# Kernel tuning notes

Measured on AMD Instinct MI355X. Metric: run time of the kernel, lower is better.

The kernel has to match this reference:

```python
import jax, jax.numpy as jnp
import numpy as np

B, S, C, H = 8, 8192, 512, 128


def setup_inputs() -> dict:
    key = jax.random.key(0)
    k1, k2 = jax.random.split(key)
    x = jax.random.normal(k1, (B, S, C), dtype=jnp.float32)
    # nn.Linear default init: U(-1/sqrt(fan_in), 1/sqrt(fan_in))
    bound = 1.0 / np.sqrt(C)
    W = jax.random.uniform(k2, (C, H), dtype=jnp.float32, minval=-bound, maxval=bound)
    b = jnp.zeros((H,), dtype=jnp.float32)
    return {"x": x, "W": W, "b": b}


def reference(x, W, b):
    # block = identity; attn = Linear(C->H) then Softmax over sequence dim (dim=1)
    logits = jnp.einsum("bsc,ch->bsh", x, W) + b          # [B, S, H]
    a = jax.nn.softmax(logits, axis=1)                     # softmax over S
    ctx = jnp.einsum("bsh,bsc->bhc", a, x)                 # a^T @ x  -> [B, H, C]
    return jnp.einsum("bsh,bhc->bsc", a, ctx)              # a @ (a^T @ x)
```

## Files before the change

kernel.cpp:

```cpp
#include <hip/hip_runtime.h>

typedef float  f32x4 __attribute__((ext_vector_type(4)));
typedef short  s16x8 __attribute__((ext_vector_type(8)));
typedef unsigned short u16;

#define OFF_E     0ULL
#define OFF_ET    16777216ULL
#define OFF_EPART 33554432ULL
#define OFF_GT    50331648ULL
#define OFF_WT    51380224ULL
#define OFF_ZP    51511296ULL
#define OFF_RZ2   51773440ULL
#define WS_NEED   51777536ULL

__device__ __forceinline__ u16 f2bf(float f) {
  unsigned u = __float_as_uint(f);
  return (u16)((u + 0x8000u) >> 16);
}
__device__ __forceinline__ unsigned pack2(float a, float b) {
  unsigned ua = __float_as_uint(a), ub = __float_as_uint(b);
  return ((ua + 0x8000u) >> 16) | ((ub + 0x8000u) & 0xffff0000u);
}

__global__ __launch_bounds__(256) void k_wt(const float* __restrict__ W,
                                            u16* __restrict__ Wt) {
  int idx = blockIdx.x * 256 + threadIdx.x;
  int h = idx & 127, c = idx >> 7;
  Wt[h * 512 + c] = f2bf(W[c * 128 + h]);
}

__global__ __launch_bounds__(256) void k_logits_e(
    const float* __restrict__ x, const u16* __restrict__ Wt,
    u16* __restrict__ e, u16* __restrict__ eT, float* __restrict__ zpart) {
  __shared__ __align__(16) u16 sm[128 * 128];
  __shared__ float zs[512];
  u16* lA = sm;
  u16* lB = sm + 8192;
  const int tid = threadIdx.x;
  const int lane = tid & 63, wave = tid >> 6;
  const int l15 = lane & 15, quad = lane >> 4;
  const int mt = blockIdx.x;
  const int rowBase = mt << 7;

  f32x4 acc[2][8];
#pragma unroll
  for (int i = 0; i < 2; ++i)
#pragma unroll
    for (int j = 0; j < 8; ++j) acc[i][j] = (f32x4){0.f, 0.f, 0.f, 0.f};

  for (int kt = 0; kt < 8; ++kt) {
    const int k0 = kt << 6;
    if (kt) __syncthreads();
    {
      const int q = tid & 3, rb = tid >> 2;
#pragma unroll
      for (int rep = 0; rep < 2; ++rep) {
        const int r = rb + rep * 64;
        const float* src = x + (size_t)(rowBase + r) * 512 + k0 + q * 4;
#pragma unroll
        for (int j = 0; j < 4; ++j) {
          f32x4 v = *(const f32x4*)(src + j * 16);
          const int chunk = (2 * j + (q >> 1)) ^ (r & 7);
          unsigned* dst = (unsigned*)&lA[r * 64 + chunk * 8 + (q & 1) * 4];
          dst[0] = pack2(v[0], v[1]);
          dst[1] = pack2(v[2], v[3]);
        }
      }
    }
    {
      const int oct = tid & 7, rb = tid >> 3;
#pragma unroll
      for (int rep = 0; rep < 4; ++rep) {
        const int r = rb + rep * 32;
        s16x8 v = *(const s16x8*)(Wt + r * 512 + k0 + oct * 8);
        *(s16x8*)&lB[r * 64 + ((oct ^ (r & 7)) * 8)] = v;
      }
    }
    __syncthreads();
#pragma unroll
    for (int kk = 0; kk < 2; ++kk) {
      s16x8 af[2], bf[8];
#pragma unroll
      for (int i = 0; i < 2; ++i) {
        const int r = wave * 32 + i * 16 + l15;
        af[i] = *(const s16x8*)&lA[r * 64 + (((kk * 4 + quad) ^ (r & 7)) * 8)];
      }
#pragma unroll
      for (int j = 0; j < 8; ++j) {
        const int r = j * 16 + l15;
        bf[j] = *(const s16x8*)&lB[r * 64 + (((kk * 4 + quad) ^ (r & 7)) * 8)];
      }
#pragma unroll
      for (int i = 0; i < 2; ++i)
#pragma unroll
        for (int j = 0; j < 8; ++j)
          acc[i][j] = __builtin_amdgcn_mfma_f32_16x16x32_bf16(af[i], bf[j], acc[i][j], 0, 0, 0);
    }
  }

  float ex[2][8][4];
  float cs[8];
#pragma unroll
  for (int j = 0; j < 8; ++j) cs[j] = 0.f;
#pragma unroll
  for (int i = 0; i < 2; ++i)
#pragma unroll
    for (int j = 0; j < 8; ++j)
#pragma unroll
      for (int rr = 0; rr < 4; ++rr) {
        float l = acc[i][j][rr];
        l = fminf(fmaxf(l, -30.f), 30.f);
        float t = __expf(l);
        ex[i][j][rr] = t;
        cs[j] += t;
      }
#pragma unroll
  for (int j = 0; j < 8; ++j) {
    cs[j] += __shfl_xor(cs[j], 16);
    cs[j] += __shfl_xor(cs[j], 32);
  }
  if (quad == 0) {
#pragma unroll
    for (int j = 0; j < 8; ++j) zs[wave * 128 + j * 16 + l15] = cs[j];
  }
  __syncthreads();

#pragma unroll
  for (int i = 0; i < 2; ++i)
#pragma unroll
    for (int j = 0; j < 8; ++j)
#pragma unroll
      for (int rr = 0; rr < 4; ++rr) {
        int s = wave * 32 + i * 16 + quad * 4 + rr;
        int h = j * 16 + l15;
        sm[s * 128 + (((h >> 3) ^ (s & 15)) * 8) + (h & 7)] = f2bf(ex[i][j][rr]);
      }
  if (tid < 128)
    zpart[mt * 128 + tid] = zs[tid] + zs[128 + tid] + zs[256 + tid] + zs[384 + tid];
  __syncthreads();

  {
    int s = tid >> 1;
#pragma unroll
    for (int i = 0; i < 8; ++i) {
      int c = (tid & 1) * 8 + i;
      s16x8 v = *(const s16x8*)&sm[s * 128 + ((c ^ (s & 15)) * 8)];
      *(s16x8*)(e + (size_t)(rowBase + s) * 128 + c * 8) = v;
    }
  }
  {
    int ck = tid & 15, hb = tid >> 4;
    int b = mt >> 6;
    int sBase = (mt & 63) << 7;
#pragma unroll
    for (int pass = 0; pass < 8; ++pass) {
      int h = hb + pass * 16;
      s16x8 v;
#pragma unroll
      for (int j = 0; j < 8; ++j) {
        int s = ck * 8 + j;
        v[j] = (short)sm[s * 128 + (((h >> 3) ^ (s & 15)) * 8) + (h & 7)];
      }
      *(s16x8*)(eT + (size_t)(b * 128 + h) * 8192 + sBase + ck * 8) = v;
    }
  }
}

__global__ __launch_bounds__(256) void k_zmerge(const float* __restrict__ zpart,
                                                float* __restrict__ rz2) {
  int gid = blockIdx.x * 256 + threadIdx.x;
  int b = gid >> 7, h = gid & 127;
  float z = 0.f;
  for (int i = 0; i < 64; ++i) z += zpart[(b * 64 + i) * 128 + h];
  rz2[gid] = 1.0f / (z * z);
}

__global__ __launch_bounds__(256) void k_E(const float* __restrict__ x,
                                           const u16* __restrict__ eT,
                                           float* __restrict__ Epart) {
  __shared__ __align__(16) u16 lA[128 * 64];
  __shared__ __align__(16) u16 lB[64 * 64];
  const int tid = threadIdx.x;
  const int lane = tid & 63, wave = tid >> 6;
  const int l15 = lane & 15, quad = lane >> 4;
  const int nt = blockIdx.x;
  const int b = blockIdx.y;
  const int kc = blockIdx.z;

  f32x4 acc[2][4];
#pragma unroll
  for (int i = 0; i < 2; ++i)
#pragma unroll
    for (int j = 0; j < 4; ++j) acc[i][j] = (f32x4){0.f, 0.f, 0.f, 0.f};

  for (int kt = 0; kt < 16; ++kt) {
    const int sb = kc * 1024 + kt * 64;
    if (kt) __syncthreads();
    {
      const int oct = tid & 7, rb = tid >> 3;
#pragma unroll
      for (int rep = 0; rep < 4; ++rep) {
        const int r = rb + rep * 32;
        s16x8 v = *(const s16x8*)(eT + (size_t)(b * 128 + r) * 8192 + sb + oct * 8);
        *(s16x8*)&lA[r * 64 + ((oct ^ (r & 7)) * 8)] = v;
      }
    }
    {
      const int cq = tid & 15, sp = tid >> 4;
#pragma unroll
      for (int p = 0; p < 2; ++p) {
        const int sl = p * 32 + sp * 2;
        const float* src = x + (size_t)(b * 8192 + sb + sl) * 512 + nt * 64 + cq * 4;
        f32x4 v0 = *(const f32x4*)src;
        f32x4 v1 = *(const f32x4*)(src + 512);
#pragma unroll
        for (int i = 0; i < 4; ++i) {
          const int c = cq * 4 + i;
          const int chunk = ((sl >> 3) & 7) ^ ((c >> 3) & 7);
          *(unsigned*)&lB[c * 64 + chunk * 8 + (sl & 7)] = pack2(v0[i], v1[i]);
        }
      }
    }
    __syncthreads();
#pragma unroll
    for (int kk = 0; kk < 2; ++kk) {
      s16x8 af[2], bf[4];
#pragma unroll
      for (int i = 0; i < 2; ++i) {
        const int r = wave * 32 + i * 16 + l15;
        af[i] = *(const s16x8*)&lA[r * 64 + (((kk * 4 + quad) ^ (r & 7)) * 8)];
      }
#pragma unroll
      for (int j = 0; j < 4; ++j) {
        const int n = j * 16 + l15;
        bf[j] = *(const s16x8*)&lB[n * 64 + (((kk * 4 + quad) ^ ((n >> 3) & 7)) * 8)];
      }
#pragma unroll
      for (int i = 0; i < 2; ++i)
#pragma unroll
        for (int j = 0; j < 4; ++j)
          acc[i][j] = __builtin_amdgcn_mfma_f32_16x16x32_bf16(af[i], bf[j], acc[i][j], 0, 0, 0);
    }
  }
  float* dst = Epart + (size_t)(kc * 8 + b) * 128 * 512 + nt * 64;
#pragma unroll
  for (int i = 0; i < 2; ++i)
#pragma unroll
    for (int j = 0; j < 4; ++j)
#pragma unroll
      for (int rr = 0; rr < 4; ++rr) {
        int h = wave * 32 + i * 16 + quad * 4 + rr;
        int c = j * 16 + l15;
        dst[(size_t)h * 512 + c] = acc[i][j][rr];
      }
}

__global__ __launch_bounds__(256) void k_G(const float* __restrict__ Epart,
                                           const float* __restrict__ rz2,
                                           u16* __restrict__ Gt) {
  int idx = blockIdx.x * 256 + threadIdx.x;
  int c = idx & 511, h = (idx >> 9) & 127, b = idx >> 16;
  float s = 0.f;
#pragma unroll
  for (int p = 0; p < 8; ++p) s += Epart[((size_t)(p * 8 + b) * 128 + h) * 512 + c];
  Gt[(size_t)(b * 512 + c) * 128 + h] = f2bf(s * rz2[b * 128 + h]);
}

__global__ __launch_bounds__(256) void k_out(const u16* __restrict__ e,
                                             const u16* __restrict__ Gt,
                                             float* __restrict__ out) {
  __shared__ __align__(16) u16 lA[128 * 128];
  __shared__ __align__(16) u16 lB[128 * 128];
  const int tid = threadIdx.x;
  const int lane = tid & 63, wave = tid >> 6;
  const int l15 = lane & 15, quad = lane >> 4;
  const int st = blockIdx.x;
  const int b = blockIdx.y;

  {
    const int hx = tid & 15, rb = tid >> 4;
#pragma unroll
    for (int pass = 0; pass < 8; ++pass) {
      const int r = rb + pass * 16;
      s16x8 v = *(const s16x8*)(e + (size_t)(b * 8192 + st * 128 + r) * 128 + hx * 8);
      *(s16x8*)&lA[r * 128 + ((hx ^ (r & 15)) * 8)] = v;
    }
  }
  for (int ct = 0; ct < 4; ++ct) {
    __syncthreads();
    {
      const int hx = tid & 15, rb = tid >> 4;
#pragma unroll
      for (int pass = 0; pass < 8; ++pass) {
        const int r = rb + pass * 16;
        s16x8 v = *(const s16x8*)(Gt + (size_t)(b * 512 + ct * 128 + r) * 128 + hx * 8);
        *(s16x8*)&lB[r * 128 + ((hx ^ (r & 15)) * 8)] = v;
      }
    }
    __syncthreads();
    f32x4 acc[2][8];
#pragma unroll
    for (int i = 0; i < 2; ++i)
#pragma unroll
      for (int j = 0; j < 8; ++j) acc[i][j] = (f32x4){0.f, 0.f, 0.f, 0.f};
#pragma unroll
    for (int kk = 0; kk < 4; ++kk) {
      s16x8 af[2], bf[8];
#pragma unroll
      for (int i = 0; i < 2; ++i) {
        const int r = wave * 32 + i * 16 + l15;
        af[i] = *(const s16x8*)&lA[r * 128 + (((kk * 4 + quad) ^ (r & 15)) * 8)];
      }
#pragma unroll
      for (int j = 0; j < 8; ++j) {
        const int n = j * 16 + l15;
        bf[j] = *(const s16x8*)&lB[n * 128 + (((kk * 4 + quad) ^ (n & 15)) * 8)];
      }
#pragma unroll
      for (int i = 0; i < 2; ++i)
#pragma unroll
        for (int j = 0; j < 8; ++j)
          acc[i][j] = __builtin_amdgcn_mfma_f32_16x16x32_bf16(af[i], bf[j], acc[i][j], 0, 0, 0);
    }
#pragma unroll
    for (int i = 0; i < 2; ++i)
#pragma unroll
      for (int j = 0; j < 8; ++j)
#pragma unroll
        for (int rr = 0; rr < 4; ++rr) {
          int s = wave * 32 + i * 16 + quad * 4 + rr;
          int c = j * 16 + l15;
          out[(size_t)(b * 8192 + st * 128 + s) * 512 + ct * 128 + c] = acc[i][j][rr];
        }
  }
}

extern "C" void kernel_launch(void* const* d_in, const int* in_sizes, int n_in,
                              void* d_out, int out_size, void* d_ws, size_t ws_size,
                              hipStream_t stream) {
  if (ws_size < (size_t)WS_NEED) return;
  const float* x = (const float*)d_in[0];
  const float* W = (const float*)d_in[1];
  float* out = (float*)d_out;
  char* ws = (char*)d_ws;
  u16* e = (u16*)(ws + OFF_E);
  u16* eT = (u16*)(ws + OFF_ET);
  float* Epart = (float*)(ws + OFF_EPART);
  u16* Gt = (u16*)(ws + OFF_GT);
  u16* Wt = (u16*)(ws + OFF_WT);
  float* zpart = (float*)(ws + OFF_ZP);
  float* rz2 = (float*)(ws + OFF_RZ2);

  k_wt<<<256, 256, 0, stream>>>(W, Wt);
  k_logits_e<<<512, 256, 0, stream>>>(x, Wt, e, eT, zpart);
  k_zmerge<<<4, 256, 0, stream>>>(zpart, rz2);
  k_E<<<dim3(8, 8, 8), 256, 0, stream>>>(x, eT, Epart);
  k_G<<<2048, 256, 0, stream>>>(Epart, rz2, Gt);
  k_out<<<dim3(64, 8), 256, 0, stream>>>(e, Gt, out);
}
```

Baseline: 306.6 us.

## Pre-transpose x to bf16 and retile the a^T·x GMEM kernel

Adds a kernel that converts x to a bf16 transposed layout [B, C, S] so that k_E loads both operands as contiguous 16-byte vectors, with no per-element fp32-to-bf16 packing or scattered LDS stores. k_E now computes 128x128 output tiles (x rows by h) over 16 split-K chunks instead of 128x64 over 8, and writes Epart in [c, h] order. k_G reduces 16 partials with vectorized loads and stores packed bf16. The cost is an extra full pass over x (read 128MB fp32, write 64MB bf16) and a larger workspace.

```diff
diff --git a/kernel.cpp b/kernel.cpp
--- a/kernel.cpp
+++ b/kernel.cpp
@@ -7,11 +7,12 @@
 #define OFF_E     0ULL
 #define OFF_ET    16777216ULL
 #define OFF_EPART 33554432ULL
-#define OFF_GT    50331648ULL
-#define OFF_WT    51380224ULL
-#define OFF_ZP    51511296ULL
-#define OFF_RZ2   51773440ULL
-#define WS_NEED   51777536ULL
+#define OFF_XT    67108864ULL
+#define OFF_GT    134217728ULL
+#define OFF_WT    135266304ULL
+#define OFF_ZP    135397376ULL
+#define OFF_RZ2   135659520ULL
+#define WS_NEED   135663616ULL
 
 __device__ __forceinline__ u16 f2bf(float f) {
   unsigned u = __float_as_uint(f);
@@ -27,6 +28,39 @@
   int idx = blockIdx.x * 256 + threadIdx.x;
   int h = idx & 127, c = idx >> 7;
   Wt[h * 512 + c] = f2bf(W[c * 128 + h]);
+}
+
+__global__ __launch_bounds__(256) void k_xT(const float* __restrict__ x,
+                                            u16* __restrict__ xT) {
+  const int tid = threadIdx.x;
+  const int sc = blockIdx.x;
+  const int b  = blockIdx.y;
+  const int rq = tid & 15;
+  const int cseg = tid >> 4;
+  const int s0 = sc * 64 + rq * 4;
+#pragma unroll
+  for (int p = 0; p < 2; ++p) {
+    const int c0 = cseg * 32 + p * 16;
+    const float* src = x + ((size_t)(b * 8192 + s0) * 512 + c0);
+    f32x4 r0[4], r1[4], r2[4], r3[4];
+#pragma unroll
+    for (int j = 0; j < 4; ++j) {
+      r0[j] = *(const f32x4*)(src + j * 4);
+      r1[j] = *(const f32x4*)(src + 512 + j * 4);
+      r2[j] = *(const f32x4*)(src + 1024 + j * 4);
+      r3[j] = *(const f32x4*)(src + 1536 + j * 4);
+    }
+#pragma unroll
+    for (int j = 0; j < 4; ++j)
+#pragma unroll
+      for (int i = 0; i < 4; ++i) {
+        const int c = c0 + j * 4 + i;
+        unsigned lo = pack2(r0[j][i], r1[j][i]);
+        unsigned hi = pack2(r2[j][i], r3[j][i]);
+        unsigned long long vv = (unsigned long long)lo | ((unsigned long long)hi << 32);
+        *(unsigned long long*)(xT + ((size_t)(b * 512 + c) * 8192 + s0)) = vv;
+      }
+  }
 }
 
 __global__ __launch_bounds__(256) void k_logits_e(
@@ -175,11 +209,11 @@
   rz2[gid] = 1.0f / (z * z);
 }
 
-__global__ __launch_bounds__(256) void k_E(const float* __restrict__ x,
+__global__ __launch_bounds__(256) void k_E(const u16* __restrict__ xT,
                                            const u16* __restrict__ eT,
                                            float* __restrict__ Epart) {
   __shared__ __align__(16) u16 lA[128 * 64];
-  __shared__ __align__(16) u16 lB[64 * 64];
+  __shared__ __align__(16) u16 lB[128 * 64];
   const int tid = threadIdx.x;
   const int lane = tid & 63, wave = tid >> 6;
   const int l15 = lane & 15, quad = lane >> 4;
@@ -187,71 +221,57 @@
   const int b = blockIdx.y;
   const int kc = blockIdx.z;
 
-  f32x4 acc[2][4];
-#pragma unroll
-  for (int i = 0; i < 2; ++i)
-#pragma unroll
-    for (int j = 0; j < 4; ++j) acc[i][j] = (f32x4){0.f, 0.f, 0.f, 0.f};
-
-  for (int kt = 0; kt < 16; ++kt) {
-    const int sb = kc * 1024 + kt * 64;
+  f32x4 acc[2][8];
+#pragma unroll
+  for (int i = 0; i < 2; ++i)
+#pragma unroll
+    for (int j = 0; j < 8; ++j) acc[i][j] = (f32x4){0.f, 0.f, 0.f, 0.f};
+
+  for (int kt = 0; kt < 8; ++kt) {
+    const int sb = kc * 512 + kt * 64;
     if (kt) __syncthreads();
     {
       const int oct = tid & 7, rb = tid >> 3;
 #pragma unroll
       for (int rep = 0; rep < 4; ++rep) {
         const int r = rb + rep * 32;
-        s16x8 v = *(const s16x8*)(eT + (size_t)(b * 128 + r) * 8192 + sb + oct * 8);
-        *(s16x8*)&lA[r * 64 + ((oct ^ (r & 7)) * 8)] = v;
-      }
-    }
-    {
-      const int cq = tid & 15, sp = tid >> 4;
-#pragma unroll
-      for (int p = 0; p < 2; ++p) {
-        const int sl = p * 32 + sp * 2;
-        const float* src = x + (size_t)(b * 8192 + sb + sl) * 512 + nt * 64 + cq * 4;
-        f32x4 v0 = *(const f32x4*)src;
-        f32x4 v1 = *(const f32x4*)(src + 512);
-#pragma unroll
-        for (int i = 0; i < 4; ++i) {
-          const int c = cq * 4 + i;
-          const int chunk = ((sl >> 3) & 7) ^ ((c >> 3) & 7);
-          *(unsigned*)&lB[c * 64 + chunk * 8 + (sl & 7)] = pack2(v0[i], v1[i]);
-        }
+        s16x8 va = *(const s16x8*)(xT + (size_t)(b * 512 + nt * 128 + r) * 8192 + sb + oct * 8);
+        *(s16x8*)&lA[r * 64 + ((oct ^ (r & 7)) * 8)] = va;
+        s16x8 vb = *(const s16x8*)(eT + (size_t)(b * 128 + r) * 8192 + sb + oct * 8);
+        *(s16x8*)&lB[r * 64 + ((oct ^ (r & 7)) * 8)] = vb;
       }
     }
     __syncthreads();
 #pragma unroll
     for (int kk = 0; kk < 2; ++kk) {
-      s16x8 af[2], bf[4];
+      s16x8 af[2], bf[8];
 #pragma unroll
       for (int i = 0; i < 2; ++i) {
         const int r = wave * 32 + i * 16 + l15;
         af[i] = *(const s16x8*)&lA[r * 64 + (((kk * 4 + quad) ^ (r & 7)) * 8)];
       }
 #pragma unroll
-      for (int j = 0; j < 4; ++j) {
+      for (int j = 0; j < 8; ++j) {
         const int n = j * 16 + l15;
-        bf[j] = *(const s16x8*)&lB[n * 64 + (((kk * 4 + quad) ^ ((n >> 3) & 7)) * 8)];
+        bf[j] = *(const s16x8*)&lB[n * 64 + (((kk * 4 + quad) ^ (n & 7)) * 8)];
       }
 #pragma unroll
       for (int i = 0; i < 2; ++i)
 #pragma unroll
-        for (int j = 0; j < 4; ++j)
+        for (int j = 0; j < 8; ++j)
           acc[i][j] = __builtin_amdgcn_mfma_f32_16x16x32_bf16(af[i], bf[j], acc[i][j], 0, 0, 0);
     }
   }
-  float* dst = Epart + (size_t)(kc * 8 + b) * 128 * 512 + nt * 64;
-#pragma unroll
-  for (int i = 0; i < 2; ++i)
-#pragma unroll
-    for (int j = 0; j < 4; ++j)
+  float* dst = Epart + ((size_t)(kc * 8 + b) * 512 + nt * 128) * 128;
+#pragma unroll
+  for (int i = 0; i < 2; ++i)
+#pragma unroll
+    for (int j = 0; j < 8; ++j)
 #pragma unroll
       for (int rr = 0; rr < 4; ++rr) {
-        int h = wave * 32 + i * 16 + quad * 4 + rr;
-        int c = j * 16 + l15;
-        dst[(size_t)h * 512 + c] = acc[i][j][rr];
+        int c = wave * 32 + i * 16 + quad * 4 + rr;
+        int h = j * 16 + l15;
+        dst[(size_t)c * 128 + h] = acc[i][j][rr];
       }
 }
 
@@ -259,11 +279,23 @@
                                            const float* __restrict__ rz2,
                                            u16* __restrict__ Gt) {
   int idx = blockIdx.x * 256 + threadIdx.x;
-  int c = idx & 511, h = (idx >> 9) & 127, b = idx >> 16;
-  float s = 0.f;
-#pragma unroll
-  for (int p = 0; p < 8; ++p) s += Epart[((size_t)(p * 8 + b) * 128 + h) * 512 + c];
-  Gt[(size_t)(b * 512 + c) * 128 + h] = f2bf(s * rz2[b * 128 + h]);
+  int h8 = idx & 15, c = (idx >> 4) & 511, b = idx >> 13;
+  f32x4 s0 = {0.f, 0.f, 0.f, 0.f}, s1 = {0.f, 0.f, 0.f, 0.f};
+#pragma unroll
+  for (int p = 0; p < 16; ++p) {
+    const float* src = Epart + (((size_t)(p * 8 + b) * 512 + c) * 128 + h8 * 8);
+    s0 += *(const f32x4*)src;
+    s1 += *(const f32x4*)(src + 4);
+  }
+  const float* rz = rz2 + b * 128 + h8 * 8;
+  f32x4 z0 = *(const f32x4*)rz;
+  f32x4 z1 = *(const f32x4*)(rz + 4);
+  unsigned ov[4];
+  ov[0] = pack2(s0[0] * z0[0], s0[1] * z0[1]);
+  ov[1] = pack2(s0[2] * z0[2], s0[3] * z0[3]);
+  ov[2] = pack2(s1[0] * z1[0], s1[1] * z1[1]);
+  ov[3] = pack2(s1[2] * z1[2], s1[3] * z1[3]);
+  *(s16x8*)(Gt + ((size_t)(b * 512 + c) * 128 + h8 * 8)) = *(s16x8*)ov;
 }
 
 __global__ __launch_bounds__(256) void k_out(const u16* __restrict__ e,
@@ -346,15 +378,17 @@
   u16* e = (u16*)(ws + OFF_E);
   u16* eT = (u16*)(ws + OFF_ET);
   float* Epart = (float*)(ws + OFF_EPART);
+  u16* xT = (u16*)(ws + OFF_XT);
   u16* Gt = (u16*)(ws + OFF_GT);
   u16* Wt = (u16*)(ws + OFF_WT);
   float* zpart = (float*)(ws + OFF_ZP);
   float* rz2 = (float*)(ws + OFF_RZ2);
 
   k_wt<<<256, 256, 0, stream>>>(W, Wt);
+  k_xT<<<dim3(128, 8), 256, 0, stream>>>(x, xT);
   k_logits_e<<<512, 256, 0, stream>>>(x, Wt, e, eT, zpart);
   k_zmerge<<<4, 256, 0, stream>>>(zpart, rz2);
-  k_E<<<dim3(8, 8, 8), 256, 0, stream>>>(x, eT, Epart);
-  k_G<<<2048, 256, 0, stream>>>(Epart, rz2, Gt);
+  k_E<<<dim3(4, 8, 16), 256, 0, stream>>>(xT, eT, Epart);
+  k_G<<<256, 256, 0, stream>>>(Epart, rz2, Gt);
   k_out<<<dim3(64, 8), 256, 0, stream>>>(e, Gt, out);
 }
```

Result: slower. 342.5 us (+11.7%).
